# Kernel tuning notes

Hardware: AMD Instinct MI355X
Metric: run time of the kernel (lower is better)

Reference implementation:

```python
import jax, jax.numpy as jnp
import numpy as np

T, A, D = 1024, 512, 128
EPS = 1e-5
NEG_SLOPE = 0.01  # torch LeakyReLU default


def setup_inputs() -> dict:
    key = jax.random.key(0)
    ks = jax.random.split(key, 5)
    return {
        "nf_task": jax.random.normal(ks[0], (T, D), dtype=jnp.float32),
        "nf_agent": jax.random.normal(ks[1], (A, D), dtype=jnp.float32),
        "W1": jax.random.normal(ks[2], (D, 2 * D), dtype=jnp.float32) * 0.05,
        "gamma1": jnp.ones((D,), dtype=jnp.float32),
        "beta1": jnp.zeros((D,), dtype=jnp.float32),
        "W2": jax.random.normal(ks[3], (1, D), dtype=jnp.float32) * 0.05,
        "gamma2": jnp.ones((1,), dtype=jnp.float32),
        "beta2": jnp.zeros((1,), dtype=jnp.float32),
        "finished": jax.random.randint(ks[4], (T,), 0, 2, dtype=jnp.int32),
    }


def reference(nf_task, nf_agent, W1, gamma1, beta1, W2, gamma2, beta2, finished):
    d = nf_task.shape[1]
    # Linear(2D->D, no bias) on concat([src, dst]) == src @ W_src^T + dst @ W_dst^T
    src_proj = nf_task @ W1[:, :d].T   # [T, D]
    dst_proj = nf_agent @ W1[:, d:].T  # [A, D]
    h = src_proj[:, None, :] + dst_proj[None, :, :]  # per-edge hidden [T, A, D]
    # BatchNorm1d(D), training mode: batch stats over all edges
    mean = h.mean(axis=(0, 1))
    var = h.var(axis=(0, 1))  # biased, as torch uses for normalization
    h = (h - mean) * jax.lax.rsqrt(var + EPS) * gamma1 + beta1
    # LeakyReLU
    h = jnp.where(h >= 0, h, NEG_SLOPE * h)
    # Linear(D->1, no bias)
    s = jnp.einsum('tad,d->ta', h, W2[0])  # [T, A]
    # BatchNorm1d(1), training mode over all edges
    m2 = s.mean()
    v2 = s.var()
    s = (s - m2) * jax.lax.rsqrt(v2 + EPS) * gamma2[0] + beta2[0]
    # mask edges whose src task is finished
    s = jnp.where(finished.astype(bool)[:, None], -jnp.inf, s)
    # reduce: each agent's mailbox = scores over incoming tasks -> policy [A, T]
    return s.T
```

## Files before the change

kernel.cpp:

```cpp
#include <hip/hip_runtime.h>
#include <math.h>

#define T_N 1024
#define A_N 512
#define D_N 128
#define EPS 1e-5f
#define LDP 132

#define WS_SP   0
#define WS_DP   131072
#define WS_PS   196608
#define WS_SQ   202752
#define WS_S2P  208896
#define WS_S2Q  209408
#define WS_C2   209920
#define WS_F2   209952
#define WS_GO   210464
#define N2F     ((float)(T_N * A_N))

#define MAGIC2 0x2468ACE1u

__device__ __forceinline__ void ast(float* p, float v) {
    __hip_atomic_store(p, v, __ATOMIC_RELAXED, __HIP_MEMORY_SCOPE_AGENT);
}
__device__ __forceinline__ float ald(const float* p) {
    return __hip_atomic_load(p, __ATOMIC_RELAXED, __HIP_MEMORY_SCOPE_AGENT);
}

__global__ __launch_bounds__(256) void ka_proj(const float* __restrict__ task,
                                               const float* __restrict__ agent,
                                               const float* __restrict__ W1,
                                               float* __restrict__ ws)
{
    __shared__ float RT[32 * LDP];
    __shared__ float WT[32 * LDP];
    __shared__ float red[256];
    int b = blockIdx.x, tid = threadIdx.x;
    int rt = b >> 2, ct = b & 3;
    bool is_t = rt < 32;
    const float* src = is_t ? task : agent;
    int woff  = is_t ? 0 : D_N;
    int rbase = (is_t ? rt : rt - 32) * 32;
    int cbase = ct * 32;

    {
        int kq = tid & 31, r0 = tid >> 5;
        for (int i = 0; i < 4; i++) {
            int row = r0 + 8 * i;
            ((float4*)(RT + row * LDP))[kq] = ((const float4*)(src + (rbase + row) * D_N))[kq];
            ((float4*)(WT + row * LDP))[kq] = ((const float4*)(W1 + (cbase + row) * (2 * D_N) + woff))[kq];
        }
    }
    __syncthreads();

    int rg = tid >> 4, cg = tid & 15;
    float a00 = 0, a01 = 0, a10 = 0, a11 = 0;
    for (int kk = 0; kk < 32; kk++) {
        float4 r0 = *(const float4*)(RT + rg * LDP + kk * 4);
        float4 r1 = *(const float4*)(RT + (rg + 16) * LDP + kk * 4);
        float4 w0 = *(const float4*)(WT + cg * LDP + kk * 4);
        float4 w1 = *(const float4*)(WT + (cg + 16) * LDP + kk * 4);
        a00 += r0.x * w0.x + r0.y * w0.y + r0.z * w0.z + r0.w * w0.w;
        a01 += r0.x * w1.x + r0.y * w1.y + r0.z * w1.z + r0.w * w1.w;
        a10 += r1.x * w0.x + r1.y * w0.y + r1.z * w0.z + r1.w * w0.w;
        a11 += r1.x * w1.x + r1.y * w1.y + r1.z * w1.z + r1.w * w1.w;
    }
    float* dst = ws + (is_t ? WS_SP : WS_DP);
    dst[(rbase + rg) * D_N + cbase + cg]           = a00;
    dst[(rbase + rg) * D_N + cbase + cg + 16]      = a01;
    dst[(rbase + rg + 16) * D_N + cbase + cg]      = a10;
    dst[(rbase + rg + 16) * D_N + cbase + cg + 16] = a11;

    float s0 = a00 + a10, s1 = a01 + a11;
    float q0 = a00 * a00 + a10 * a10, q1 = a01 * a01 + a11 * a11;
    for (int off = 16; off <= 32; off <<= 1) {
        s0 += __shfl_xor(s0, off); s1 += __shfl_xor(s1, off);
        q0 += __shfl_xor(q0, off); q1 += __shfl_xor(q1, off);
    }
    int wid = tid >> 6, lane = tid & 63;
    if (lane < 16) {
        red[wid * 64 + lane]      = s0;
        red[wid * 64 + 16 + lane] = s1;
        red[wid * 64 + 32 + lane] = q0;
        red[wid * 64 + 48 + lane] = q1;
    }
    __syncthreads();
    if (tid < 64) {
        float v = red[tid] + red[64 + tid] + red[128 + tid] + red[192 + tid];
        int base = (tid < 32) ? WS_PS : WS_SQ;
        ws[base + rt * 128 + cbase + (tid & 31)] = v;
    }
}

__global__ __launch_bounds__(256) void kb_sweep(const float* __restrict__ g1,
                                                const float* __restrict__ b1,
                                                const float* __restrict__ W2,
                                                const float* __restrict__ g2,
                                                const float* __restrict__ b2,
                                                const int* __restrict__ fin,
                                                float* __restrict__ ws,
                                                float* __restrict__ out)
{
    __shared__ float spT[32 * LDP];
    __shared__ float dpT[32 * LDP];
    __shared__ float scs[128], shs[128];
    __shared__ float w9s[128];
    __shared__ float Pl[32], Ql[32];
    __shared__ float stile[32 * 36];
    __shared__ float red[512];

    const int b = blockIdx.x, tid = threadIdx.x;
    const int bx = b & 31, by = b >> 5;
    const int rowbase = bx * 32, colbase = by * 32;
    unsigned* flags = (unsigned*)(ws + WS_F2);
    unsigned* go    = (unsigned*)(ws + WS_GO);

    if (tid < 128) {
        float as = 0.f, ds = 0.f;
        for (int r = 0;  r < 32; r++) as += ws[WS_PS + r * 128 + tid];
        for (int r = 32; r < 48; r++) ds += ws[WS_PS + r * 128 + tid];
        red[tid] = as; red[128 + tid] = ds;
        w9s[tid] = 0.495f * W2[tid];
    } else {
        int j = tid - 128;
        float aq = 0.f, dq = 0.f;
        for (int r = 0;  r < 32; r++) aq += ws[WS_SQ + r * 128 + j];
        for (int r = 32; r < 48; r++) dq += ws[WS_SQ + r * 128 + j];
        red[256 + j] = aq; red[384 + j] = dq;
    }
    __syncthreads();
    if (tid < 128) {
        float ms = red[tid] * (1.f / T_N);
        float md = red[128 + tid] * (1.f / A_N);
        float var = red[256 + tid] * (1.f / T_N) - ms * ms
                  + red[384 + tid] * (1.f / A_N) - md * md;
        float s = g1[tid] * rsqrtf(var + EPS);
        scs[tid] = s;
        shs[tid] = b1[tid] - (ms + md) * s;
    }
    __syncthreads();

    {
        int k = (tid & 31) * 4, r8 = tid >> 5;
        float4 sc4 = *(const float4*)(scs + k);
        float4 sh4 = *(const float4*)(shs + k);
        for (int it = 0; it < 4; it++) {
            int t = it * 8 + r8;
            float4 v = *(const float4*)(ws + WS_SP + (rowbase + t) * D_N + k);
            v.x *= sc4.x; v.y *= sc4.y; v.z *= sc4.z; v.w *= sc4.w;
            *(float4*)(spT + t * LDP + k) = v;
        }
        for (int it = 0; it < 4; it++) {
            int a = it * 8 + r8;
            float4 v = *(const float4*)(ws + WS_DP + (colbase + a) * D_N + k);
            v.x = v.x * sc4.x + sh4.x; v.y = v.y * sc4.y + sh4.y;
            v.z = v.z * sc4.z + sh4.z; v.w = v.w * sc4.w + sh4.w;
            *(float4*)(dpT + a * LDP + k) = v;
        }
    }
    __syncthreads();

    {
        int row = tid >> 3, seg = tid & 7;
        float p = 0.f, q = 0.f;
        for (int c = 0; c < 4; c++) {
            int kk = seg * 16 + c * 4;
            float4 wv = *(const float4*)(W2 + kk);
            float4 sv = *(const float4*)(spT + row * LDP + kk);
            float4 dv = *(const float4*)(dpT + row * LDP + kk);
            p += wv.x * sv.x + wv.y * sv.y + wv.z * sv.z + wv.w * sv.w;
            q += wv.x * dv.x + wv.y * dv.y + wv.z * dv.z + wv.w * dv.w;
        }
        for (int off = 1; off <= 4; off <<= 1) {
            p += __shfl_xor(p, off);
            q += __shfl_xor(q, off);
        }
        if (seg == 0) { Pl[row] = 0.505f * p; Ql[row] = 0.505f * q; }
    }
    __syncthreads();

    int tx = tid & 15, ty = tid >> 4;
    float a00 = 0, a01 = 0, a10 = 0, a11 = 0;
    #pragma unroll 4
    for (int kk = 0; kk < 32; kk++) {
        float4 w9 = *(const float4*)(w9s + kk * 4);
        float4 s0 = *(const float4*)(spT + ty * LDP + kk * 4);
        float4 s1 = *(const float4*)(spT + (ty + 16) * LDP + kk * 4);
        float4 d0 = *(const float4*)(dpT + tx * LDP + kk * 4);
        float4 d1 = *(const float4*)(dpT + (tx + 16) * LDP + kk * 4);
        float u;
        u = s0.x + d0.x; a00 = fmaf(w9.x, fabsf(u), a00);
        u = s0.y + d0.y; a00 = fmaf(w9.y, fabsf(u), a00);
        u = s0.z + d0.z; a00 = fmaf(w9.z, fabsf(u), a00);
        u = s0.w + d0.w; a00 = fmaf(w9.w, fabsf(u), a00);
        u = s0.x + d1.x; a01 = fmaf(w9.x, fabsf(u), a01);
        u = s0.y + d1.y; a01 = fmaf(w9.y, fabsf(u), a01);
        u = s0.z + d1.z; a01 = fmaf(w9.z, fabsf(u), a01);
        u = s0.w + d1.w; a01 = fmaf(w9.w, fabsf(u), a01);
        u = s1.x + d0.x; a10 = fmaf(w9.x, fabsf(u), a10);
        u = s1.y + d0.y; a10 = fmaf(w9.y, fabsf(u), a10);
        u = s1.z + d0.z; a10 = fmaf(w9.z, fabsf(u), a10);
        u = s1.w + d0.w; a10 = fmaf(w9.w, fabsf(u), a10);
        u = s1.x + d1.x; a11 = fmaf(w9.x, fabsf(u), a11);
        u = s1.y + d1.y; a11 = fmaf(w9.y, fabsf(u), a11);
        u = s1.z + d1.z; a11 = fmaf(w9.z, fabsf(u), a11);
        u = s1.w + d1.w; a11 = fmaf(w9.w, fabsf(u), a11);
    }
    {
        float p0 = Pl[ty], p1 = Pl[ty + 16];
        float q0 = Ql[tx], q1 = Ql[tx + 16];
        a00 += p0 + q0; a01 += p0 + q1;
        a10 += p1 + q0; a11 += p1 + q1;
    }

    {
        float lsum = a00 + a01 + a10 + a11;
        float lsq  = a00 * a00 + a01 * a01 + a10 * a10 + a11 * a11;
        stile[tx * 36 + ty]              = a00;
        stile[(tx + 16) * 36 + ty]       = a01;
        stile[tx * 36 + ty + 16]         = a10;
        stile[(tx + 16) * 36 + ty + 16]  = a11;
        for (int off = 1; off <= 32; off <<= 1) {
            lsum += __shfl_xor(lsum, off);
            lsq  += __shfl_xor(lsq,  off);
        }
        int wid = tid >> 6;
        if ((tid & 63) == 0) { red[wid] = lsum; red[8 + wid] = lsq; }
        __syncthreads();
        if (tid == 0) {
            ast(ws + WS_S2P + b, red[0] + red[1] + red[2] + red[3]);
            ast(ws + WS_S2Q + b, red[8] + red[9] + red[10] + red[11]);
        }
    }

    __syncthreads();
    if (tid == 0)
        __hip_atomic_store(&flags[b], MAGIC2, __ATOMIC_RELAXED, __HIP_MEMORY_SCOPE_AGENT);
    if (b == 0) {
        while (__hip_atomic_load(&flags[tid], __ATOMIC_RELAXED, __HIP_MEMORY_SCOPE_AGENT) != MAGIC2 ||
               __hip_atomic_load(&flags[tid + 256], __ATOMIC_RELAXED, __HIP_MEMORY_SCOPE_AGENT) != MAGIC2)
            __builtin_amdgcn_s_sleep(1);
        __syncthreads();
        float v1 = ald(ws + WS_S2P + tid) + ald(ws + WS_S2P + 256 + tid);
        float v2 = ald(ws + WS_S2Q + tid) + ald(ws + WS_S2Q + 256 + tid);
        for (int off = 1; off <= 32; off <<= 1) {
            v1 += __shfl_xor(v1, off);
            v2 += __shfl_xor(v2, off);
        }
        if ((tid & 63) == 0) { red[tid >> 6] = v1; red[8 + (tid >> 6)] = v2; }
        __syncthreads();
        if (tid == 0) {
            float s2s = red[0] + red[1] + red[2] + red[3];
            float s2q = red[8] + red[9] + red[10] + red[11];
            float m2   = s2s / N2F;
            float var2 = s2q / N2F - m2 * m2;
            float sc2 = g2[0] * rsqrtf(var2 + EPS);
            ast(ws + WS_C2,     sc2);
            ast(ws + WS_C2 + 1, b2[0] - m2 * sc2);
            __hip_atomic_store(go, MAGIC2, __ATOMIC_RELEASE, __HIP_MEMORY_SCOPE_AGENT);
        }
    }
    if (tid == 0)
        while (__hip_atomic_load(go, __ATOMIC_RELAXED, __HIP_MEMORY_SCOPE_AGENT) != MAGIC2)
            __builtin_amdgcn_s_sleep(4);
    __syncthreads();

    {
        if (tid == 0) { red[0] = ald(ws + WS_C2); red[1] = ald(ws + WS_C2 + 1); }
        __syncthreads();
        float sc2 = red[0], sh2 = red[1];
        const float NEG = -1.0e38f;
        int j4 = (tid & 7) * 4, a = tid >> 3;
        int4 f = *(const int4*)(fin + rowbase + j4);
        float4 v = *(const float4*)(stile + a * 36 + j4);
        float4 o;
        o.x = f.x ? NEG : v.x * sc2 + sh2;
        o.y = f.y ? NEG : v.y * sc2 + sh2;
        o.z = f.z ? NEG : v.z * sc2 + sh2;
        o.w = f.w ? NEG : v.w * sc2 + sh2;
        *(float4*)(out + (colbase + a) * T_N + rowbase + j4) = o;
    }
}

extern "C" void kernel_launch(void* const* d_in, const int* in_sizes, int n_in,
                              void* d_out, int out_size, void* d_ws, size_t ws_size,
                              hipStream_t stream) {
    (void)in_sizes; (void)n_in; (void)out_size; (void)ws_size;
    const float* task  = (const float*)d_in[0];
    const float* agent = (const float*)d_in[1];
    const float* W1    = (const float*)d_in[2];
    const float* g1    = (const float*)d_in[3];
    const float* b1    = (const float*)d_in[4];
    const float* W2    = (const float*)d_in[5];
    const float* g2    = (const float*)d_in[6];
    const float* b2    = (const float*)d_in[7];
    const int*   fin   = (const int*)d_in[8];

    ka_proj<<<192, 256, 0, stream>>>(task, agent, W1, (float*)d_ws);
    kb_sweep<<<512, 256, 0, stream>>>(g1, b1, W2, g2, b2, fin, (float*)d_ws, (float*)d_out);
}
```

Baseline: 86.79 us.

## Finalize BatchNorm1 stats in last projection block, prefetch projection tiles in sweep

A per-column-tile atomic counter in ka_proj lets the last finishing block reduce the partial sums and sumsq and write the BatchNorm1 scale and shift to the workspace. Previously every one of the 512 kb_sweep blocks re-reduced all 48 partial rows redundantly. kb_sweep now just loads the finished scale and shift, issues its src and dst projection loads into registers up front, and spins with a shorter sleep. The counter check assumes the workspace starts at a specific poison value (0xAAAAAAAA) and is never reset, so correctness depends on the harness re-poisoning the workspace before each call.

```diff
diff --git a/kernel.cpp b/kernel.cpp
--- a/kernel.cpp
+++ b/kernel.cpp
@@ -16,9 +16,13 @@
 #define WS_C2   209920
 #define WS_F2   209952
 #define WS_GO   210464
+#define WS_SCS  210468
+#define WS_SHS  210596
+#define WS_CNT  210724
 #define N2F     ((float)(T_N * A_N))
 
 #define MAGIC2 0x2468ACE1u
+#define POISON 0xAAAAAAAAu
 
 __device__ __forceinline__ void ast(float* p, float v) {
     __hip_atomic_store(p, v, __ATOMIC_RELAXED, __HIP_MEMORY_SCOPE_AGENT);
@@ -30,11 +34,14 @@
 __global__ __launch_bounds__(256) void ka_proj(const float* __restrict__ task,
                                                const float* __restrict__ agent,
                                                const float* __restrict__ W1,
+                                               const float* __restrict__ g1,
+                                               const float* __restrict__ b1,
                                                float* __restrict__ ws)
 {
     __shared__ float RT[32 * LDP];
     __shared__ float WT[32 * LDP];
     __shared__ float red[256];
+    __shared__ unsigned lastf;
     int b = blockIdx.x, tid = threadIdx.x;
     int rt = b >> 2, ct = b & 3;
     bool is_t = rt < 32;
@@ -88,13 +95,39 @@
     if (tid < 64) {
         float v = red[tid] + red[64 + tid] + red[128 + tid] + red[192 + tid];
         int base = (tid < 32) ? WS_PS : WS_SQ;
-        ws[base + rt * 128 + cbase + (tid & 31)] = v;
-    }
-}
-
-__global__ __launch_bounds__(256) void kb_sweep(const float* __restrict__ g1,
-                                                const float* __restrict__ b1,
-                                                const float* __restrict__ W2,
+        ast(ws + base + rt * 128 + cbase + (tid & 31), v);
+    }
+    __syncthreads();
+    if (tid == 0) {
+        unsigned old = atomicAdd((unsigned*)(ws + WS_CNT) + ct, 1u);
+        lastf = (old == POISON + 47u) ? 1u : 0u;
+    }
+    __syncthreads();
+    if (lastf) {
+        if (tid < 64) {
+            int c = tid & 31, which = tid >> 5;
+            int base = which ? WS_SQ : WS_PS;
+            float aT = 0.f, aA = 0.f;
+            for (int r = 0;  r < 32; r++) aT += ald(ws + base + r * 128 + cbase + c);
+            for (int r = 32; r < 48; r++) aA += ald(ws + base + r * 128 + cbase + c);
+            red[which * 64 + c]      = aT;
+            red[which * 64 + 32 + c] = aA;
+        }
+        __syncthreads();
+        if (tid < 32) {
+            int j = cbase + tid;
+            float ms = red[tid]      * (1.f / T_N);
+            float md = red[32 + tid] * (1.f / A_N);
+            float var = red[64 + tid] * (1.f / T_N) - ms * ms
+                      + red[96 + tid] * (1.f / A_N) - md * md;
+            float s = g1[j] * rsqrtf(var + EPS);
+            ws[WS_SCS + j] = s;
+            ws[WS_SHS + j] = b1[j] - (ms + md) * s;
+        }
+    }
+}
+
+__global__ __launch_bounds__(256) void kb_sweep(const float* __restrict__ W2,
                                                 const float* __restrict__ g2,
                                                 const float* __restrict__ b2,
                                                 const int* __restrict__ fin,
@@ -115,47 +148,31 @@
     unsigned* flags = (unsigned*)(ws + WS_F2);
     unsigned* go    = (unsigned*)(ws + WS_GO);
 
+    const int kq = (tid & 31) * 4, r8 = tid >> 5;
+    float4 sraw[4], draw[4];
+    for (int it = 0; it < 4; it++) {
+        sraw[it] = *(const float4*)(ws + WS_SP + (rowbase + it * 8 + r8) * D_N + kq);
+        draw[it] = *(const float4*)(ws + WS_DP + (colbase + it * 8 + r8) * D_N + kq);
+    }
     if (tid < 128) {
-        float as = 0.f, ds = 0.f;
-        for (int r = 0;  r < 32; r++) as += ws[WS_PS + r * 128 + tid];
-        for (int r = 32; r < 48; r++) ds += ws[WS_PS + r * 128 + tid];
-        red[tid] = as; red[128 + tid] = ds;
+        scs[tid] = ws[WS_SCS + tid];
+        shs[tid] = ws[WS_SHS + tid];
         w9s[tid] = 0.495f * W2[tid];
-    } else {
-        int j = tid - 128;
-        float aq = 0.f, dq = 0.f;
-        for (int r = 0;  r < 32; r++) aq += ws[WS_SQ + r * 128 + j];
-        for (int r = 32; r < 48; r++) dq += ws[WS_SQ + r * 128 + j];
-        red[256 + j] = aq; red[384 + j] = dq;
-    }
-    __syncthreads();
-    if (tid < 128) {
-        float ms = red[tid] * (1.f / T_N);
-        float md = red[128 + tid] * (1.f / A_N);
-        float var = red[256 + tid] * (1.f / T_N) - ms * ms
-                  + red[384 + tid] * (1.f / A_N) - md * md;
-        float s = g1[tid] * rsqrtf(var + EPS);
-        scs[tid] = s;
-        shs[tid] = b1[tid] - (ms + md) * s;
-    }
-    __syncthreads();
-
-    {
-        int k = (tid & 31) * 4, r8 = tid >> 5;
-        float4 sc4 = *(const float4*)(scs + k);
-        float4 sh4 = *(const float4*)(shs + k);
+    }
+    __syncthreads();
+
+    {
+        float4 sc4 = *(const float4*)(scs + kq);
+        float4 sh4 = *(const float4*)(shs + kq);
         for (int it = 0; it < 4; it++) {
             int t = it * 8 + r8;
-            float4 v = *(const float4*)(ws + WS_SP + (rowbase + t) * D_N + k);
+            float4 v = sraw[it];
             v.x *= sc4.x; v.y *= sc4.y; v.z *= sc4.z; v.w *= sc4.w;
-            *(float4*)(spT + t * LDP + k) = v;
-        }
-        for (int it = 0; it < 4; it++) {
-            int a = it * 8 + r8;
-            float4 v = *(const float4*)(ws + WS_DP + (colbase + a) * D_N + k);
-            v.x = v.x * sc4.x + sh4.x; v.y = v.y * sc4.y + sh4.y;
-            v.z = v.z * sc4.z + sh4.z; v.w = v.w * sc4.w + sh4.w;
-            *(float4*)(dpT + a * LDP + k) = v;
+            *(float4*)(spT + t * LDP + kq) = v;
+            float4 w = draw[it];
+            w.x = w.x * sc4.x + sh4.x; w.y = w.y * sc4.y + sh4.y;
+            w.z = w.z * sc4.z + sh4.z; w.w = w.w * sc4.w + sh4.w;
+            *(float4*)(dpT + t * LDP + kq) = w;
         }
     }
     __syncthreads();
@@ -262,7 +279,7 @@
     }
     if (tid == 0)
         while (__hip_atomic_load(go, __ATOMIC_RELAXED, __HIP_MEMORY_SCOPE_AGENT) != MAGIC2)
-            __builtin_amdgcn_s_sleep(4);
+            __builtin_amdgcn_s_sleep(1);
     __syncthreads();
 
     {
@@ -296,6 +313,6 @@
     const float* b2    = (const float*)d_in[7];
     const int*   fin   = (const int*)d_in[8];
 
-    ka_proj<<<192, 256, 0, stream>>>(task, agent, W1, (float*)d_ws);
-    kb_sweep<<<512, 256, 0, stream>>>(g1, b1, W2, g2, b2, fin, (float*)d_ws, (float*)d_out);
-}
+    ka_proj<<<192, 256, 0, stream>>>(task, agent, W1, g1, b1, (float*)d_ws);
+    kb_sweep<<<512, 256, 0, stream>>>(W2, g2, b2, fin, (float*)d_ws, (float*)d_out);
+}
```

Measured after the change: 87.50 us. No clear change (+0.8%).
